# Performance work log

Measured on AMD Instinct MI355X. Metric: run time of the kernel, lower is better.

## Reference

```python
import jax, jax.numpy as jnp
import numpy as np

B, N, D = 1024, 7, 1024
SQRT_D = float(np.sqrt(D))
MAX_CTX, MAX_VIB = 0.24, 0.26
VIB_IDX, CTX_IDX = 3, N - 1

ADJ = jnp.asarray(np.array([
    [1, 1, 0, 0, 1, 1, 1],
    [1, 1, 1, 1, 1, 1, 1],
    [0, 1, 1, 0, 1, 0, 1],
    [0, 1, 0, 1, 1, 1, 1],
    [1, 1, 1, 1, 1, 1, 1],
    [1, 1, 0, 1, 1, 1, 1],
    [1, 1, 1, 1, 1, 1, 1]], dtype=np.float32))


def _gelu(x):
    return jax.nn.gelu(x, approximate=False)


def setup_inputs() -> dict:
    key = jax.random.key(0)
    ks = jax.random.split(key, 20)
    s = 0.02
    def w(k, shape):
        return jax.random.normal(k, shape, dtype=jnp.float32) * s
    return {
        "nodes": jax.random.normal(ks[0], (B, N, D), dtype=jnp.float32),
        "Wq": w(ks[1], (D, D)), "bq": jnp.zeros((D,), jnp.float32),
        "Wk": w(ks[2], (D, D)), "bk": jnp.zeros((D,), jnp.float32),
        "Wv": w(ks[3], (D, D)), "bv": jnp.zeros((D,), jnp.float32),
        "We1": w(ks[4], (3 * D, D)), "be1": jnp.zeros((D,), jnp.float32),
        "We2": w(ks[5], (D, 1)), "be2": jnp.zeros((1,), jnp.float32),
        "Wu1": w(ks[6], (2 * D, D)), "bu1": jnp.zeros((D,), jnp.float32),
        "Wu2": w(ks[7], (D, D)), "bu2": jnp.zeros((D,), jnp.float32),
        "Wi1": w(ks[8], (2 * D, D)), "bi1": jnp.zeros((D,), jnp.float32),
        "Wi2": w(ks[9], (D, 1)), "bi2": jnp.zeros((1,), jnp.float32),
    }


def _cap_importance(imp):
    cap = jnp.ones((N,), imp.dtype).at[VIB_IDX].set(MAX_VIB).at[CTX_IDX].set(MAX_CTX)
    free = jnp.ones((N,), imp.dtype).at[VIB_IDX].set(0.0).at[CTX_IDX].set(0.0)[None, :]
    capped = jnp.minimum(imp, cap[None, :])
    free_mass = (imp * free).sum(axis=1, keepdims=True)
    residual = jnp.clip(1.0 - capped.sum(axis=1, keepdims=True), 0.0)
    uniform = free / jnp.maximum(free.sum(axis=1, keepdims=True), 1.0)
    free_share = jnp.where(free_mass > 1e-6,
                           imp * free / jnp.maximum(free_mass, 1e-6),
                           uniform)
    redis = capped + free_share * residual
    return redis / jnp.maximum(redis.sum(axis=1, keepdims=True), 1e-6)


def _physics_loss(upd):
    norms = jnp.linalg.norm(upd, axis=-1)  # [B,N]
    dots = jnp.einsum('bnd,bmd->bnm', upd, upd)
    cos = dots / jnp.maximum(norms[:, :, None] * norms[:, None, :], 1e-8)
    eye = jnp.eye(N, dtype=upd.dtype)
    edge_loss = ((1.0 - cos) * ADJ[None]).sum() / jnp.maximum(ADJ.sum() * upd.shape[0], 1.0) * upd.shape[0]
    # note: torch sums over batch too -> divide by ADJ.sum() only
    edge_loss = ((1.0 - cos) * ADJ[None]).sum() / jnp.maximum(ADJ.sum(), 1.0)
    non_mask = (1.0 - ADJ) * (1.0 - eye)
    non_loss = (jax.nn.relu(cos - 0.35) * non_mask[None]).sum() / jnp.maximum(non_mask.sum(), 1.0)
    return edge_loss + 0.5 * non_loss


def _alignment_loss(upd, fused):
    fn = fused / jnp.maximum(jnp.linalg.norm(fused, axis=-1, keepdims=True), 1e-12)
    nn_ = upd / jnp.maximum(jnp.linalg.norm(upd, axis=-1, keepdims=True), 1e-12)
    cos = jnp.einsum('bnd,bd->bn', nn_, fn)
    return (1.0 - cos).mean()


def reference(nodes, Wq, bq, Wk, bk, Wv, bv, We1, be1, We2, be2,
              Wu1, bu1, Wu2, bu2, Wi1, bi1, Wi2, bi2):
    q = nodes @ Wq + bq
    k = nodes @ Wk + bk
    v = nodes @ Wv + bv
    logits = jnp.einsum('bnd,bmd->bnm', q, k) / SQRT_D
    # edge gate: cat([left, right, ctx]) @ We1 == left@Wa + right@Wb + ctx@Wc
    Wa, Wb, Wc = We1[:D], We1[D:2 * D], We1[2 * D:]
    la = nodes @ Wa                      # [B,N,D] (left varies over axis n)
    rb = nodes @ Wb                      # [B,N,D] (right varies over axis m)
    cc = nodes[:, -1] @ Wc               # [B,D]   (ctx broadcast)
    h = la[:, :, None, :] + rb[:, None, :, :] + cc[:, None, None, :] + be1
    edge_logits = (_gelu(h) @ We2 + be2)[..., 0]  # [B,N,N]
    masked = logits + edge_logits + (ADJ[None] - 1.0) * 10000.0
    attn = jax.nn.softmax(masked, axis=-1)
    messages = jnp.einsum('bnm,bmd->bnd', attn, v)
    upd_in = jnp.concatenate([nodes, messages], axis=-1)
    updated = _gelu(upd_in @ Wu1 + bu1) @ Wu2 + bu2 + nodes
    gq = jnp.broadcast_to(updated[:, -1:, :], updated.shape)
    imp_in = jnp.concatenate([updated, gq], axis=-1)
    imp_logits = (_gelu(imp_in @ Wi1 + bi1) @ Wi2 + bi2)[..., 0]
    imp = jax.nn.softmax(imp_logits, axis=-1)
    imp = _cap_importance(imp)
    fused = jnp.einsum('bn,bnd->bd', imp, updated)
    phys = _physics_loss(updated)
    align = _alignment_loss(updated, fused)
    return (fused, updated, imp, attn, phys + align * 0.0, align)
```

## Files before the change

kernel.cpp:

```cpp
#include <hip/hip_runtime.h>
#include <hip/hip_bf16.h>


typedef __attribute__((ext_vector_type(8))) short bf16x8;
typedef __attribute__((ext_vector_type(4))) float f32x4;
typedef __attribute__((ext_vector_type(16))) float f32x16;

__constant__ float c_adj[49] = {
    1,1,0,0,1,1,1,
    1,1,1,1,1,1,1,
    0,1,1,0,1,0,1,
    0,1,0,1,1,1,1,
    1,1,1,1,1,1,1,
    1,1,0,1,1,1,1,
    1,1,1,1,1,1,1};

__device__ __forceinline__ float gelu_f(float x) {
    float z = fabsf(x) * 0.70710678118654752f;
    float t = 1.0f / (1.0f + 0.3275911f * z);
    float poly = ((((1.061405429f * t - 1.453152027f) * t + 1.421413741f) * t
                  - 0.284496736f) * t + 0.254829592f) * t;
    float e = __expf(-z * z);
    float erf_abs = 1.0f - poly * e;
    float erf = copysignf(erf_abs, x);
    return 0.5f * x * (1.0f + erf);
}
__device__ __forceinline__ float b2f(unsigned short u) {
    unsigned int x = ((unsigned int)u) << 16;
    union { unsigned int i; float f; } c; c.i = x; return c.f;
}
__device__ __forceinline__ unsigned short f2b(float f) {
    __hip_bfloat16 h = __float2bfloat16(f);
    union { __hip_bfloat16 b; unsigned short u; } c; c.b = h; return c.u;
}

__device__ __forceinline__ void gload_lds16(const void* g, void* l) {
    __builtin_amdgcn_global_load_lds(
        (const __attribute__((address_space(1))) unsigned int*)g,
        (__attribute__((address_space(3))) unsigned int*)l, 16, 0, 0);
}

__device__ __forceinline__ int maprow(int r, int mode) {
    if (mode == 1) return r * 7 + 6;
    if (mode == 2) return r - r % 7 + 6;
    return r;
}

__global__ __launch_bounds__(256) void gemm128w32(
    const unsigned short* __restrict__ A1, int a1Mode,
    const unsigned short* __restrict__ A2, int a2Mode,
    const unsigned short* __restrict__ WT, int ldw,
    const float* __restrict__ bias,
    const float* __restrict__ resid,
    float* __restrict__ Cf,
    unsigned short* __restrict__ Cb, size_t segStride,
    int K, int act)
{
    __shared__ short As[3][128 * 32];
    __shared__ short Bs[3][128 * 32];
    const int tid = threadIdx.x;
    const int lane = tid & 63;
    const int w = tid >> 6;
    const int wr = (w >> 1) * 64;
    const int wc = (w & 1) * 64;

    int lin = blockIdx.y * gridDim.x + blockIdx.x;
    const int nwg = gridDim.x * gridDim.y;
    const int cpx = nwg >> 3;
    lin = (lin & 7) * cpx + (lin >> 3);
    const int row0 = (lin / gridDim.x) * 128;
    const int col0 = (lin % gridDim.x) * 128;

    const int l31 = lane & 31;
    const int hi  = lane >> 5;
    const int xorv = (l31 >> 1) & 3;
    int aRow[2], bRow[2], cOff[2];
    aRow[0] = (wr + l31) * 32;       aRow[1] = (wr + 32 + l31) * 32;
    bRow[0] = (wc + l31) * 32;       bRow[1] = (wc + 32 + l31) * 32;
    cOff[0] = ((hi)     ^ xorv) * 8;
    cOff[1] = ((2 + hi) ^ xorv) * 8;

    const int NTt = K >> 5;

    auto stage = [&](int ktn) {
        int k0n = ktn * 32;
        const unsigned short* srcA; int mode; int kbase;
        if (k0n < 1024) { srcA = A1; mode = a1Mode; kbase = k0n; }
        else            { srcA = A2; mode = a2Mode; kbase = k0n - 1024; }
        int slot = ktn % 3;
        #pragma unroll
        for (int rnd = 0; rnd < 2; ++rnd) {
            int c2 = rnd * 256 + tid;
            int m = c2 >> 2, ch = c2 & 3;
            int kc = (ch ^ ((m >> 1) & 3)) * 8;
            int rr = maprow(row0 + m, mode);
            gload_lds16(srcA + (size_t)rr * 1024 + kbase + kc, &As[slot][c2 * 8]);
        }
        #pragma unroll
        for (int rnd = 0; rnd < 2; ++rnd) {
            int c2 = rnd * 256 + tid;
            int n = c2 >> 2, ch = c2 & 3;
            int kc = (ch ^ ((n >> 1) & 3)) * 8;
            gload_lds16(WT + (size_t)(col0 + n) * ldw + k0n + kc, &Bs[slot][c2 * 8]);
        }
    };

    f32x16 acc[2][2] = {};

    stage(0);
    if (NTt > 1) stage(1);
    asm volatile("s_waitcnt vmcnt(4)" ::: "memory");
    asm volatile("s_barrier" ::: "memory");

    for (int kt = 0; kt < NTt; ++kt) {
        const short* Ab = &As[kt % 3][0];
        const short* Bb = &Bs[kt % 3][0];

        if (kt + 2 < NTt) stage(kt + 2);

        bf16x8 af[2][2], bfv[2][2];
        #pragma unroll
        for (int ks = 0; ks < 2; ++ks) {
            #pragma unroll
            for (int mf = 0; mf < 2; ++mf)
                af[mf][ks] = *(const bf16x8*)(Ab + aRow[mf] + cOff[ks]);
            #pragma unroll
            for (int nf = 0; nf < 2; ++nf)
                bfv[nf][ks] = *(const bf16x8*)(Bb + bRow[nf] + cOff[ks]);
        }

        __builtin_amdgcn_s_setprio(1);
        #pragma unroll
        for (int ks = 0; ks < 2; ++ks)
            #pragma unroll
            for (int mf = 0; mf < 2; ++mf)
                #pragma unroll
                for (int nf = 0; nf < 2; ++nf)
                    acc[mf][nf] = __builtin_amdgcn_mfma_f32_32x32x16_bf16(
                        af[mf][ks], bfv[nf][ks], acc[mf][nf], 0, 0, 0);
        __builtin_amdgcn_s_setprio(0);

        if (kt < NTt - 2) asm volatile("s_waitcnt vmcnt(4)" ::: "memory");
        else              asm volatile("s_waitcnt vmcnt(0)" ::: "memory");
        asm volatile("s_barrier" ::: "memory");
    }

    #pragma unroll
    for (int mf = 0; mf < 2; ++mf) {
        #pragma unroll
        for (int nf = 0; nf < 2; ++nf) {
            int c = col0 + wc + nf * 32 + l31;
            float bv = bias ? bias[c] : 0.0f;
            int seg = c >> 10, c0 = c & 1023;
            #pragma unroll
            for (int r = 0; r < 16; ++r) {
                int row = row0 + wr + mf * 32 + (r & 3) + 8 * (r >> 2) + 4 * hi;
                float vv = acc[mf][nf][r] + bv;
                if (act) vv = gelu_f(vv);
                if (resid) vv += resid[(size_t)row * 1024 + c];
                if (Cf) Cf[(size_t)row * 1024 + c] = vv;
                if (Cb) Cb[(size_t)seg * segStride + (size_t)row * 1024 + c0] = f2b(vv);
            }
        }
    }
}

__global__ __launch_bounds__(256) void gemm64x128(
    const unsigned short* __restrict__ A1, int a1Mode,
    const unsigned short* __restrict__ A2, int a2Mode,
    const unsigned short* __restrict__ WT, int ldw,
    const float* __restrict__ bias,
    const float* __restrict__ resid,
    float* __restrict__ Cf,
    unsigned short* __restrict__ Cb,
    int K, int act)
{
    __shared__ short As[64 * 32];
    __shared__ short Bs[128 * 32];
    const int tid = threadIdx.x;
    const int lane = tid & 63;
    const int w = tid >> 6;
    const int wc = w * 32;
    const int row0 = blockIdx.y * 64;
    const int col0 = blockIdx.x * 128;
    const int fr = lane & 15;
    const int fko = (((lane >> 4) ^ ((fr >> 1) & 3)) << 3);

    f32x4 acc[4][2] = {};

    for (int k0 = 0; k0 < K; k0 += 32) {
        const unsigned short* srcA; int mode; int kbase;
        if (k0 < 1024) { srcA = A1; mode = a1Mode; kbase = k0; }
        else           { srcA = A2; mode = a2Mode; kbase = k0 - 1024; }
        {
            int m = tid >> 2, ch = tid & 3;
            int kc = (ch ^ ((m >> 1) & 3)) * 8;
            int rr = maprow(row0 + m, mode);
            gload_lds16(srcA + (size_t)rr * 1024 + kbase + kc, &As[tid * 8]);
        }
        #pragma unroll
        for (int rnd = 0; rnd < 2; ++rnd) {
            int c = rnd * 256 + tid;
            int n = c >> 2, ch = c & 3;
            int kc = (ch ^ ((n >> 1) & 3)) * 8;
            gload_lds16(WT + (size_t)(col0 + n) * ldw + k0 + kc, &Bs[c * 8]);
        }
        __syncthreads();
        bf16x8 af[4], bf_[2];
        #pragma unroll
        for (int i = 0; i < 4; ++i)
            af[i] = *(const bf16x8*)(&As[(i * 16 + fr) * 32 + fko]);
        #pragma unroll
        for (int j = 0; j < 2; ++j)
            bf_[j] = *(const bf16x8*)(&Bs[(wc + j * 16 + fr) * 32 + fko]);
        #pragma unroll
        for (int i = 0; i < 4; ++i)
            #pragma unroll
            for (int j = 0; j < 2; ++j)
                acc[i][j] = __builtin_amdgcn_mfma_f32_16x16x32_bf16(
                    af[i], bf_[j], acc[i][j], 0, 0, 0);
        __syncthreads();
    }

    const int qrow = (lane >> 4) * 4;
    const int qcol = lane & 15;
    #pragma unroll
    for (int i = 0; i < 4; ++i) {
        int rbase = row0 + i * 16 + qrow;
        #pragma unroll
        for (int j = 0; j < 2; ++j) {
            int c = col0 + wc + j * 16 + qcol;
            float bv = bias ? bias[c] : 0.0f;
            #pragma unroll
            for (int reg = 0; reg < 4; ++reg) {
                int r = rbase + reg;
                float vv = acc[i][j][reg] + bv;
                if (act) vv = gelu_f(vv);
                if (resid) vv += resid[(size_t)r * 1024 + c];
                if (Cf) Cf[(size_t)r * 1024 + c] = vv;
                if (Cb) Cb[(size_t)r * 1024 + c] = f2b(vv);
            }
        }
    }
}

__global__ __launch_bounds__(256) void cast_f2b(
    const float* __restrict__ in, unsigned short* __restrict__ out, int n)
{
    int i = (blockIdx.x * 256 + threadIdx.x) * 4;
    if (i >= n) return;
    float4 v = *(const float4*)(in + i);
    ushort4 o;
    o.x = f2b(v.x); o.y = f2b(v.y); o.z = f2b(v.z); o.w = f2b(v.w);
    *(ushort4*)(out + i) = o;
}

__global__ __launch_bounds__(256) void tcast_all(
    const float* __restrict__ Wq, const float* __restrict__ Wk,
    const float* __restrict__ Wv, const float* __restrict__ We1,
    const float* __restrict__ Wu1, const float* __restrict__ Wu2,
    const float* __restrict__ Wi1,
    unsigned short* __restrict__ WT_all, unsigned short* __restrict__ Wu1T,
    unsigned short* __restrict__ Wu2T, unsigned short* __restrict__ Wi1T)
{
    const int z = blockIdx.z;
    const float* src; unsigned short* dst; int R;
    switch (z) {
        case 0: src = Wq;            dst = WT_all;               R = 1024; break;
        case 1: src = Wk;            dst = WT_all + 1024 * 1024; R = 1024; break;
        case 2: src = Wv;            dst = WT_all + 2048 * 1024; R = 1024; break;
        case 3: src = We1;           dst = WT_all + 3072 * 1024; R = 1024; break;
        case 4: src = We1 + 1048576; dst = WT_all + 4096 * 1024; R = 1024; break;
        case 5: src = We1 + 2097152; dst = WT_all + 5120 * 1024; R = 1024; break;
        case 6: src = Wu1;           dst = Wu1T;                 R = 2048; break;
        case 7: src = Wu2;           dst = Wu2T;                 R = 1024; break;
        default: src = Wi1;          dst = Wi1T;                 R = 2048; break;
    }
    const int rt = blockIdx.y * 32;
    if (rt >= R) return;
    const int ct = blockIdx.x * 32;
    __shared__ float t[32][33];
    const int tx = threadIdx.x & 31, ty = threadIdx.x >> 5;
    #pragma unroll
    for (int s = 0; s < 4; ++s)
        t[ty + s * 8][tx] = src[(size_t)(rt + ty + s * 8) * 1024 + ct + tx];
    __syncthreads();
    #pragma unroll
    for (int s = 0; s < 4; ++s)
        dst[(size_t)(ct + ty + s * 8) * R + rt + tx] = f2b(t[tx][ty + s * 8]);
}

__global__ void build_bias(const float* __restrict__ bq,
                           const float* __restrict__ bk,
                           const float* __restrict__ bv,
                           float* __restrict__ bias_all,
                           float* __restrict__ acc)
{
    int i = blockIdx.x * 256 + threadIdx.x;
    if (i < 4) acc[i] = 0.f;
    if (i >= 5120) return;
    int seg = i >> 10, c = i & 1023;
    float v = 0.f;
    if (seg == 0) v = bq[c];
    else if (seg == 1) v = bk[c];
    else if (seg == 2) v = bv[c];
    bias_all[i] = v;
}

__global__ __launch_bounds__(256) void attn_msg_b(
    const unsigned short* __restrict__ q, const unsigned short* __restrict__ k,
    const unsigned short* __restrict__ v,
    const unsigned short* __restrict__ la, const unsigned short* __restrict__ rb,
    const float* __restrict__ cc,
    const float* __restrict__ We2, const float* __restrict__ be2,
    float* __restrict__ attn_out, unsigned short* __restrict__ msg)
{
    const int bn = blockIdx.x;
    const int b = bn / 7, n = bn % 7;
    const int tid = threadIdx.x;
    const int lane = tid & 63, wv = tid >> 6;
    const int d0 = tid * 4;
    __shared__ float red[4][14];
    __shared__ float sm[7];

    float qv[4], lav[4], wev[4];
    {
        ushort4 q4 = *(const ushort4*)(q + (size_t)bn * 1024 + d0);
        ushort4 l4 = *(const ushort4*)(la + (size_t)bn * 1024 + d0);
        float4 c4 = *(const float4*)(cc + (size_t)b * 1024 + d0);
        float4 w4 = *(const float4*)(We2 + d0);
        qv[0] = b2f(q4.x); qv[1] = b2f(q4.y); qv[2] = b2f(q4.z); qv[3] = b2f(q4.w);
        lav[0] = b2f(l4.x) + c4.x; lav[1] = b2f(l4.y) + c4.y;
        lav[2] = b2f(l4.z) + c4.z; lav[3] = b2f(l4.w) + c4.w;
        wev[0] = w4.x; wev[1] = w4.y; wev[2] = w4.z; wev[3] = w4.w;
    }

    float s1a[7], s2a[7];
    #pragma unroll
    for (int m = 0; m < 7; ++m) {
        ushort4 k4 = *(const ushort4*)(k  + (size_t)(b * 7 + m) * 1024 + d0);
        ushort4 r4 = *(const ushort4*)(rb + (size_t)(b * 7 + m) * 1024 + d0);
        s1a[m] = qv[0] * b2f(k4.x) + qv[1] * b2f(k4.y)
               + qv[2] * b2f(k4.z) + qv[3] * b2f(k4.w);
        s2a[m] = gelu_f(lav[0] + b2f(r4.x)) * wev[0]
               + gelu_f(lav[1] + b2f(r4.y)) * wev[1]
               + gelu_f(lav[2] + b2f(r4.z)) * wev[2]
               + gelu_f(lav[3] + b2f(r4.w)) * wev[3];
    }
    #pragma unroll
    for (int m = 0; m < 7; ++m) {
        float x1 = s1a[m], x2 = s2a[m];
        #pragma unroll
        for (int off = 32; off > 0; off >>= 1) {
            x1 += __shfl_down(x1, off);
            x2 += __shfl_down(x2, off);
        }
        if (lane == 0) { red[wv][m] = x1; red[wv][7 + m] = x2; }
    }
    __syncthreads();
    if (tid == 0) {
        float l[7];
        #pragma unroll
        for (int m = 0; m < 7; ++m) {
            float d1 = red[0][m] + red[1][m] + red[2][m] + red[3][m];
            float d2 = red[0][7 + m] + red[1][7 + m] + red[2][7 + m] + red[3][7 + m];
            l[m] = d1 * (1.0f / 32.0f) + d2 + be2[0]
                 + (c_adj[n * 7 + m] - 1.0f) * 10000.0f;
        }
        float mx = l[0];
        #pragma unroll
        for (int m = 1; m < 7; ++m) mx = fmaxf(mx, l[m]);
        float e[7], s = 0.f;
        #pragma unroll
        for (int m = 0; m < 7; ++m) { e[m] = __expf(l[m] - mx); s += e[m]; }
        float inv = 1.0f / s;
        #pragma unroll
        for (int m = 0; m < 7; ++m) {
            float wgt = e[m] * inv;
            sm[m] = wgt;
            attn_out[(size_t)bn * 7 + m] = wgt;
        }
    }
    __syncthreads();
    float wr_[7];
    #pragma unroll
    for (int m = 0; m < 7; ++m) wr_[m] = sm[m];
    float s0 = 0.f, s1 = 0.f, s2 = 0.f, s3 = 0.f;
    #pragma unroll
    for (int m = 0; m < 7; ++m) {
        ushort4 v4 = *(const ushort4*)(v + (size_t)(b * 7 + m) * 1024 + d0);
        s0 += wr_[m] * b2f(v4.x); s1 += wr_[m] * b2f(v4.y);
        s2 += wr_[m] * b2f(v4.z); s3 += wr_[m] * b2f(v4.w);
    }
    ushort4 o;
    o.x = f2b(s0); o.y = f2b(s1); o.z = f2b(s2); o.w = f2b(s3);
    *(ushort4*)(msg + (size_t)bn * 1024 + d0) = o;
}

__global__ __launch_bounds__(256) void row_dot_b(
    const unsigned short* __restrict__ H, const float* __restrict__ w2,
    const float* __restrict__ b2, float* __restrict__ out)
{
    const int r = blockIdx.x;
    const int tid = threadIdx.x;
    const int lane = tid & 63, wv = tid >> 6;
    __shared__ float red[4];
    const int d0 = tid * 4;
    ushort4 h4 = *(const ushort4*)(H + (size_t)r * 1024 + d0);
    float4 w4 = *(const float4*)(w2 + d0);
    float s = b2f(h4.x) * w4.x + b2f(h4.y) * w4.y
            + b2f(h4.z) * w4.z + b2f(h4.w) * w4.w;
    #pragma unroll
    for (int off = 32; off > 0; off >>= 1) s += __shfl_down(s, off);
    if (lane == 0) red[wv] = s;
    __syncthreads();
    if (tid == 0) out[r] = red[0] + red[1] + red[2] + red[3] + b2[0];
}

__global__ __launch_bounds__(256) void imp_fused_k(
    const float* __restrict__ logits, const float* __restrict__ upd,
    float* __restrict__ imp_out, float* __restrict__ fused_out)
{
    const int b = blockIdx.x;
    const int tid = threadIdx.x;
    __shared__ float w[7];
    if (tid == 0) {
        float l[7], e[7];
        float mx = -1e30f;
        for (int i = 0; i < 7; ++i) { l[i] = logits[b * 7 + i]; mx = fmaxf(mx, l[i]); }
        float s = 0.f;
        for (int i = 0; i < 7; ++i) { e[i] = expf(l[i] - mx); s += e[i]; }
        float inv = 1.0f / s;
        float imp[7];
        for (int i = 0; i < 7; ++i) imp[i] = e[i] * inv;
        const float cap[7] = {1.f, 1.f, 1.f, 0.26f, 1.f, 1.f, 0.24f};
        const float fr[7]  = {1.f, 1.f, 1.f, 0.f,   1.f, 1.f, 0.f};
        float capped[7], capsum = 0.f, fmass = 0.f;
        for (int i = 0; i < 7; ++i) {
            capped[i] = fminf(imp[i], cap[i]);
            capsum += capped[i];
            fmass += imp[i] * fr[i];
        }
        float residual = fmaxf(1.0f - capsum, 0.0f);
        float redis[7], rs = 0.f;
        for (int i = 0; i < 7; ++i) {
            float fs = (fmass > 1e-6f) ? imp[i] * fr[i] / fmaxf(fmass, 1e-6f)
                                       : fr[i] * 0.2f;
            redis[i] = capped[i] + fs * residual;
            rs += redis[i];
        }
        float invr = 1.0f / fmaxf(rs, 1e-6f);
        for (int i = 0; i < 7; ++i) {
            float wi = redis[i] * invr;
            w[i] = wi;
            imp_out[b * 7 + i] = wi;
        }
    }
    __syncthreads();
    float wr[7];
    #pragma unroll
    for (int i = 0; i < 7; ++i) wr[i] = w[i];
    #pragma unroll
    for (int j = 0; j < 4; ++j) {
        int d = tid + j * 256;
        float s = 0.f;
        #pragma unroll
        for (int nn2 = 0; nn2 < 7; ++nn2)
            s += wr[nn2] * upd[(size_t)(b * 7 + nn2) * 1024 + d];
        fused_out[(size_t)b * 1024 + d] = s;
    }
}

__global__ __launch_bounds__(256) void physics_k(
    const float* __restrict__ upd, const float* __restrict__ fused,
    float* __restrict__ accums)
{
    const int b = blockIdx.x;
    const int tid = threadIdx.x;
    const int lane = tid & 63, wv = tid >> 6;
    __shared__ float u[7][1024];
    __shared__ float f[1024];
    __shared__ float wred[4][36];
    for (int idx = tid; idx < 7 * 1024; idx += 256)
        u[idx >> 10][idx & 1023] = upd[(size_t)b * 7168 + idx];
    for (int d = tid; d < 1024; d += 256)
        f[d] = fused[(size_t)b * 1024 + d];
    __syncthreads();

    float vals[36];
    #pragma unroll
    for (int i = 0; i < 36; ++i) vals[i] = 0.f;
    for (int d = tid; d < 1024; d += 256) {
        float x[7];
        #pragma unroll
        for (int n = 0; n < 7; ++n) x[n] = u[n][d];
        float fv = f[d];
        int idx = 0;
        #pragma unroll
        for (int n = 0; n < 7; ++n) {
            #pragma unroll
            for (int m = n; m < 7; ++m) vals[idx++] += x[n] * x[m];
        }
        #pragma unroll
        for (int n = 0; n < 7; ++n) vals[28 + n] += x[n] * fv;
        vals[35] += fv * fv;
    }
    #pragma unroll
    for (int i = 0; i < 36; ++i) {
        float s = vals[i];
        #pragma unroll
        for (int off = 32; off > 0; off >>= 1) s += __shfl_down(s, off);
        if (lane == 0) wred[wv][i] = s;
    }
    __syncthreads();
    if (tid == 0) {
        float tv[36];
        for (int i = 0; i < 36; ++i)
            tv[i] = wred[0][i] + wred[1][i] + wred[2][i] + wred[3][i];
        auto didx = [](int n, int m) -> int {
            if (n > m) { int t = n; n = m; m = t; }
            return n * 7 - n * (n - 1) / 2 + (m - n);
        };
        float norms[7];
        for (int n = 0; n < 7; ++n) norms[n] = sqrtf(tv[didx(n, n)]);
        float e = 0.f, nl = 0.f;
        for (int n = 0; n < 7; ++n)
            for (int m = 0; m < 7; ++m) {
                float cos_ = tv[didx(n, m)] / fmaxf(norms[n] * norms[m], 1e-8f);
                float adj = c_adj[n * 7 + m];
                e += (1.0f - cos_) * adj;
                if (adj == 0.0f && n != m) nl += fmaxf(cos_ - 0.35f, 0.0f);
            }
        float fnorm = sqrtf(tv[35]);
        float al = 0.f;
        for (int n = 0; n < 7; ++n) {
            float cosn = tv[28 + n] /
                         (fmaxf(norms[n], 1e-12f) * fmaxf(fnorm, 1e-12f));
            al += 1.0f - cosn;
        }
        atomicAdd(&accums[0], e);
        atomicAdd(&accums[1], nl);
        atomicAdd(&accums[2], al);
    }
}

__global__ void finalize_k(const float* __restrict__ a,
                           float* __restrict__ phys_o,
                           float* __restrict__ align_o)
{
    phys_o[0]  = a[0] / 41.0f + 0.5f * (a[1] / 8.0f);
    align_o[0] = a[2] * (1.0f / 7168.0f);
}

extern "C" void kernel_launch(void* const* d_in, const int* in_sizes, int n_in,
                              void* d_out, int out_size, void* d_ws, size_t ws_size,
                              hipStream_t stream)
{
    const float* nodes = (const float*)d_in[0];
    const float* Wq  = (const float*)d_in[1];
    const float* bq  = (const float*)d_in[2];
    const float* Wk  = (const float*)d_in[3];
    const float* bk  = (const float*)d_in[4];
    const float* Wv  = (const float*)d_in[5];
    const float* bv  = (const float*)d_in[6];
    const float* We1 = (const float*)d_in[7];
    const float* be1 = (const float*)d_in[8];
    const float* We2 = (const float*)d_in[9];
    const float* be2 = (const float*)d_in[10];
    const float* Wu1 = (const float*)d_in[11];
    const float* bu1 = (const float*)d_in[12];
    const float* Wu2 = (const float*)d_in[13];
    const float* bu2 = (const float*)d_in[14];
    const float* Wi1 = (const float*)d_in[15];
    const float* bi1 = (const float*)d_in[16];
    const float* Wi2 = (const float*)d_in[17];
    const float* bi2 = (const float*)d_in[18];

    float* out = (float*)d_out;
    float* fused_o = out;
    float* upd_o   = out + 1048576;
    float* imp_o   = out + 1048576 + 7340032;
    float* attn_o  = imp_o + 7168;
    float* phys_o  = attn_o + 50176;
    float* align_o = phys_o + 1;

    const size_t BIG = 7340032;
    const size_t MEG = 1048576;
    char* p = (char*)d_ws;
    unsigned short* nodes_b = (unsigned short*)p; p += BIG * 2;
    unsigned short* qb      = (unsigned short*)p; p += BIG * 2;
    unsigned short* kb      = (unsigned short*)p; p += BIG * 2;
    unsigned short* vb      = (unsigned short*)p; p += BIG * 2;
    unsigned short* lab     = (unsigned short*)p; p += BIG * 2;
    unsigned short* rbb     = (unsigned short*)p; p += BIG * 2;
    unsigned short* WT_all  = (unsigned short*)p; p += (size_t)6144 * 1024 * 2;
    unsigned short* Wu1T    = (unsigned short*)p; p += 2 * MEG * 2;
    unsigned short* Wu2T    = (unsigned short*)p; p += MEG * 2;
    unsigned short* Wi1T    = (unsigned short*)p; p += 2 * MEG * 2;
    float* bias_all = (float*)p; p += 5120 * 4;
    float* ccf = (float*)p; p += MEG * 4;
    float* il  = (float*)p; p += 7168 * 4;
    float* acc = (float*)p; p += 4 * 4;
    unsigned short* msgb = lab;
    unsigned short* hub  = qb;
    unsigned short* updb = kb;
    unsigned short* hib  = vb;

    dim3 blk(256);

    cast_f2b<<<dim3(7168), blk, 0, stream>>>(nodes, nodes_b, 7340032);
    tcast_all<<<dim3(32, 64, 9), blk, 0, stream>>>(Wq, Wk, Wv, We1, Wu1, Wu2, Wi1,
                                                   WT_all, Wu1T, Wu2T, Wi1T);
    build_bias<<<dim3(20), blk, 0, stream>>>(bq, bk, bv, bias_all, acc);

    gemm128w32<<<dim3(40, 56), blk, 0, stream>>>(
        nodes_b, 0, nullptr, 0, WT_all, 1024, bias_all, nullptr,
        nullptr, qb, BIG, 1024, 0);

    gemm64x128<<<dim3(8, 16), blk, 0, stream>>>(
        nodes_b, 1, nullptr, 0, WT_all + (size_t)5120 * 1024, 1024, be1, nullptr,
        ccf, nullptr, 1024, 0);

    attn_msg_b<<<dim3(7168), blk, 0, stream>>>(qb, kb, vb, lab, rbb, ccf, We2, be2,
                                               attn_o, msgb);

    gemm128w32<<<dim3(8, 56), blk, 0, stream>>>(
        nodes_b, 0, msgb, 0, Wu1T, 2048, bu1, nullptr, nullptr, hub, 0, 2048, 1);
    gemm128w32<<<dim3(8, 56), blk, 0, stream>>>(
        hub, 0, nullptr, 0, Wu2T, 1024, bu2, nodes, upd_o, updb, 0, 1024, 0);
    gemm128w32<<<dim3(8, 56), blk, 0, stream>>>(
        updb, 0, updb, 2, Wi1T, 2048, bi1, nullptr, nullptr, hib, 0, 2048, 1);

    row_dot_b<<<dim3(7168), blk, 0, stream>>>(hib, Wi2, bi2, il);
    imp_fused_k<<<dim3(1024), blk, 0, stream>>>(il, upd_o, imp_o, fused_o);
    physics_k<<<dim3(1024), blk, 0, stream>>>(upd_o, fused_o, acc);
    finalize_k<<<1, 1, 0, stream>>>(acc, phys_o, align_o);
}
```

Baseline: 580.8 us.

## Fuse importance and physics kernels, strengthen LDS swizzle in GEMM

The importance softmax and fused-sum kernel is merged with the physics-loss kernel, so the updated rows are loaded into shared memory once and the fused vector stays in LDS rather than being written out and read back. This removes one launch and a second global read of the updated tensor. The GEMM shared-memory XOR swizzle now also mixes in higher row bits, aiming to cut LDS bank conflicts on the fragment reads. The fused kernel keeps the same large shared-memory footprint, so occupancy is unchanged.

```diff
diff --git a/kernel.cpp b/kernel.cpp
--- a/kernel.cpp
+++ b/kernel.cpp
@@ -73,7 +73,7 @@
 
     const int l31 = lane & 31;
     const int hi  = lane >> 5;
-    const int xorv = (l31 >> 1) & 3;
+    const int xorv = ((l31 >> 1) ^ (l31 >> 3)) & 3;
     int aRow[2], bRow[2], cOff[2];
     aRow[0] = (wr + l31) * 32;       aRow[1] = (wr + 32 + l31) * 32;
     bRow[0] = (wc + l31) * 32;       bRow[1] = (wc + 32 + l31) * 32;
@@ -92,7 +92,7 @@
         for (int rnd = 0; rnd < 2; ++rnd) {
             int c2 = rnd * 256 + tid;
             int m = c2 >> 2, ch = c2 & 3;
-            int kc = (ch ^ ((m >> 1) & 3)) * 8;
+            int kc = (ch ^ (((m >> 1) ^ (m >> 3)) & 3)) * 8;
             int rr = maprow(row0 + m, mode);
             gload_lds16(srcA + (size_t)rr * 1024 + kbase + kc, &As[slot][c2 * 8]);
         }
@@ -100,7 +100,7 @@
         for (int rnd = 0; rnd < 2; ++rnd) {
             int c2 = rnd * 256 + tid;
             int n = c2 >> 2, ch = c2 & 3;
-            int kc = (ch ^ ((n >> 1) & 3)) * 8;
+            int kc = (ch ^ (((n >> 1) ^ (n >> 3)) & 3)) * 8;
             gload_lds16(WT + (size_t)(col0 + n) * ldw + k0n + kc, &Bs[slot][c2 * 8]);
         }
     };
@@ -417,13 +417,22 @@
     if (tid == 0) out[r] = red[0] + red[1] + red[2] + red[3] + b2[0];
 }
 
-__global__ __launch_bounds__(256) void imp_fused_k(
+__global__ __launch_bounds__(256) void imp_phys_k(
     const float* __restrict__ logits, const float* __restrict__ upd,
-    float* __restrict__ imp_out, float* __restrict__ fused_out)
+    float* __restrict__ imp_out, float* __restrict__ fused_out,
+    float* __restrict__ accums)
 {
     const int b = blockIdx.x;
     const int tid = threadIdx.x;
-    __shared__ float w[7];
+    const int lane = tid & 63, wv = tid >> 6;
+    __shared__ float u[7][1024];
+    __shared__ float f[1024];
+    __shared__ float wsh[7];
+    __shared__ float wred[4][36];
+
+    for (int idx = tid; idx < 7 * 1024; idx += 256)
+        u[idx >> 10][idx & 1023] = upd[(size_t)b * 7168 + idx];
+
     if (tid == 0) {
         float l[7], e[7];
         float mx = -1e30f;
@@ -452,39 +461,25 @@
         float invr = 1.0f / fmaxf(rs, 1e-6f);
         for (int i = 0; i < 7; ++i) {
             float wi = redis[i] * invr;
-            w[i] = wi;
+            wsh[i] = wi;
             imp_out[b * 7 + i] = wi;
         }
     }
     __syncthreads();
+
     float wr[7];
     #pragma unroll
-    for (int i = 0; i < 7; ++i) wr[i] = w[i];
+    for (int i = 0; i < 7; ++i) wr[i] = wsh[i];
     #pragma unroll
     for (int j = 0; j < 4; ++j) {
         int d = tid + j * 256;
         float s = 0.f;
         #pragma unroll
         for (int nn2 = 0; nn2 < 7; ++nn2)
-            s += wr[nn2] * upd[(size_t)(b * 7 + nn2) * 1024 + d];
+            s += wr[nn2] * u[nn2][d];
+        f[d] = s;
         fused_out[(size_t)b * 1024 + d] = s;
     }
-}
-
-__global__ __launch_bounds__(256) void physics_k(
-    const float* __restrict__ upd, const float* __restrict__ fused,
-    float* __restrict__ accums)
-{
-    const int b = blockIdx.x;
-    const int tid = threadIdx.x;
-    const int lane = tid & 63, wv = tid >> 6;
-    __shared__ float u[7][1024];
-    __shared__ float f[1024];
-    __shared__ float wred[4][36];
-    for (int idx = tid; idx < 7 * 1024; idx += 256)
-        u[idx >> 10][idx & 1023] = upd[(size_t)b * 7168 + idx];
-    for (int d = tid; d < 1024; d += 256)
-        f[d] = fused[(size_t)b * 1024 + d];
     __syncthreads();
 
     float vals[36];
@@ -632,7 +627,6 @@
         updb, 0, updb, 2, Wi1T, 2048, bi1, nullptr, nullptr, hib, 0, 2048, 1);
 
     row_dot_b<<<dim3(7168), blk, 0, stream>>>(hib, Wi2, bi2, il);
-    imp_fused_k<<<dim3(1024), blk, 0, stream>>>(il, upd_o, imp_o, fused_o);
-    physics_k<<<dim3(1024), blk, 0, stream>>>(upd_o, fused_o, acc);
+    imp_phys_k<<<dim3(1024), blk, 0, stream>>>(il, upd_o, imp_o, fused_o, acc);
     finalize_k<<<1, 1, 0, stream>>>(acc, phys_o, align_o);
 }
```

Result: no change. 580.2 us (-0.1%).
